# Kernel tuning notes

Hardware: AMD Instinct MI355X
Metric: run time of the kernel (lower is better)

Reference implementation:

```python
import jax, jax.numpy as jnp
import numpy as np

N_NODES = 100000
N_EDGES = 1600000
IN_CH, HID1, HID2, HID3, OUT_CH = 128, 64, 64, 256, 64


def gcn_conv(x, W, b, src, dst, n_nodes):
    """PyG GCNConv: linear transform, add self-loops, symmetric-normalized aggregation."""
    h = x @ W  # [N, d_out]
    # degree at target nodes, counting the self-loop (+1)
    deg = jnp.zeros((n_nodes,), dtype=h.dtype).at[dst].add(1.0) + 1.0
    dinv = jax.lax.rsqrt(deg)  # deg >= 1, safe
    norm = dinv[src] * dinv[dst]  # [E]
    # scatter-add normalized messages from src to dst
    agg = jnp.zeros_like(h).at[dst].add(h[src] * norm[:, None])
    # self-loop contribution: norm_ii = dinv[i]^2
    agg = agg + h * (dinv * dinv)[:, None]
    return agg + b


def setup_inputs() -> dict:
    key = jax.random.key(0)
    ks = jax.random.split(key, 8)
    x = jax.random.normal(ks[0], (N_NODES, IN_CH), dtype=jnp.float32)
    edge_index = jax.random.randint(ks[1], (2, N_EDGES), 0, N_NODES, dtype=jnp.int64)
    def glorot(k, fan_in, fan_out):
        s = jnp.sqrt(6.0 / (fan_in + fan_out)).astype(jnp.float32)
        return jax.random.uniform(k, (fan_in, fan_out), jnp.float32, -s, s)
    return {
        "x": x,
        "edge_index": edge_index,
        "W1": glorot(ks[2], IN_CH, HID1), "b1": jnp.zeros((HID1,), jnp.float32),
        "W2": glorot(ks[3], HID1, HID2), "b2": jnp.zeros((HID2,), jnp.float32),
        "W3": glorot(ks[4], HID2, HID3), "b3": jnp.zeros((HID3,), jnp.float32),
        "W4": glorot(ks[5], HID3, OUT_CH), "b4": jnp.zeros((OUT_CH,), jnp.float32),
    }


def reference(x, edge_index, W1, b1, W2, b2, W3, b3, W4, b4):
    src, dst = edge_index[0], edge_index[1]
    n = x.shape[0]
    h = jax.nn.relu(gcn_conv(x, W1, b1, src, dst, n))
    h = jax.nn.relu(gcn_conv(h, W2, b2, src, dst, n))
    h = h @ W3 + b3  # hidden Linear (no activation, per original forward)
    h = h @ W4 + b4  # output Linear
    return jax.nn.log_softmax(h, axis=-1)
```

## Files before the change

kernel.cpp:

```cpp
#include <hip/hip_runtime.h>
#include <hip/hip_bf16.h>
#include <math.h>

#define NNODES 100000
#define NEDGES 1600000
#define NB 782
#define PB 256
#define EPB 6250
#define SCAN_N (NB * PB)
#define CAP 4608

typedef __bf16 bf16x8 __attribute__((ext_vector_type(8)));
typedef float f32x4 __attribute__((ext_vector_type(4)));
typedef unsigned int u32x4 __attribute__((ext_vector_type(4)));

static __device__ inline unsigned short f2bf(float f) {
    __hip_bfloat16 h = __float2bfloat16(f);
    return *reinterpret_cast<unsigned short*>(&h);
}


__global__ __launch_bounds__(256) void hist_kernel(const int* __restrict__ dst,
                                                   int* __restrict__ histg) {
    __shared__ int h[NB];
    int tid = threadIdx.x, blk = blockIdx.x;
    for (int b = tid; b < NB; b += 256) h[b] = 0;
    __syncthreads();
    int base = blk * EPB;
    for (int i = base + tid; i < base + EPB; i += 256)
        atomicAdd(&h[dst[i] >> 7], 1);
    __syncthreads();
    for (int b = tid; b < NB; b += 256) histg[b * PB + blk] = h[b];
}


__global__ __launch_bounds__(256) void scan1_kernel(const int* __restrict__ cnt,
                                                    int* __restrict__ off,
                                                    int* __restrict__ bsum, int n) {
    __shared__ int tmp[256];
    int tid = threadIdx.x;
    int t4 = blockIdx.x * 1024 + tid * 4;
    int v0 = (t4 + 0 < n) ? cnt[t4 + 0] : 0;
    int v1 = (t4 + 1 < n) ? cnt[t4 + 1] : 0;
    int v2 = (t4 + 2 < n) ? cnt[t4 + 2] : 0;
    int v3 = (t4 + 3 < n) ? cnt[t4 + 3] : 0;
    int ssum = v0 + v1 + v2 + v3;
    tmp[tid] = ssum;
    __syncthreads();
    for (int d = 1; d < 256; d <<= 1) {
        int x = (tid >= d) ? tmp[tid - d] : 0;
        __syncthreads();
        tmp[tid] += x;
        __syncthreads();
    }
    int run = tmp[tid] - ssum;
    if (t4 + 0 < n) off[t4 + 0] = run; run += v0;
    if (t4 + 1 < n) off[t4 + 1] = run; run += v1;
    if (t4 + 2 < n) off[t4 + 2] = run; run += v2;
    if (t4 + 3 < n) off[t4 + 3] = run;
    if (tid == 255) bsum[blockIdx.x] = tmp[255];
}

__global__ __launch_bounds__(256) void scan2_kernel(const int* __restrict__ bsum,
                                                    int* __restrict__ bsum_ex, int nb) {
    __shared__ int tmp[256];
    int tid = threadIdx.x;
    int v = (tid < nb) ? bsum[tid] : 0;
    tmp[tid] = v;
    __syncthreads();
    for (int d = 1; d < 256; d <<= 1) {
        int x = (tid >= d) ? tmp[tid - d] : 0;
        __syncthreads();
        tmp[tid] += x;
        __syncthreads();
    }
    bsum_ex[tid] = tmp[tid] - v;
}

__global__ __launch_bounds__(256) void scan3t_kernel(const int* __restrict__ part_scan,
                                                     const int* __restrict__ bsum_ex,
                                                     const int* __restrict__ histg,
                                                     int* __restrict__ gbaseT,
                                                     int* __restrict__ cntT, int n) {
    int i = blockIdx.x * 256 + threadIdx.x;
    if (i < n) {
        int v = part_scan[i] + bsum_ex[i >> 10];
        int b = i >> 8, blk = i & 255;
        gbaseT[blk * NB + b] = v;
        cntT[blk * NB + b] = histg[i];
    }
}


__global__ __launch_bounds__(256) void part_kernel(const int* __restrict__ src,
                                                   const int* __restrict__ dst,
                                                   const int* __restrict__ gbaseT,
                                                   const int* __restrict__ cntT,
                                                   unsigned int* __restrict__ part) {
    __shared__ unsigned int sorted[EPB];
    __shared__ int gaddr[EPB];
    __shared__ int gcol[NB];
    __shared__ int base_l[NB];
    __shared__ int cur[NB];
    __shared__ int tmp[256];
    int tid = threadIdx.x, blk = blockIdx.x;
    for (int b = tid; b < NB; b += 256) {
        gcol[b] = gbaseT[blk * NB + b];
        base_l[b] = cntT[blk * NB + b];
        cur[b] = 0;
    }
    __syncthreads();
    int t4 = tid * 4;
    int v0 = (t4 + 0 < NB) ? base_l[t4 + 0] : 0;
    int v1 = (t4 + 1 < NB) ? base_l[t4 + 1] : 0;
    int v2 = (t4 + 2 < NB) ? base_l[t4 + 2] : 0;
    int v3 = (t4 + 3 < NB) ? base_l[t4 + 3] : 0;
    int ssum = v0 + v1 + v2 + v3;
    tmp[tid] = ssum;
    __syncthreads();
    for (int d = 1; d < 256; d <<= 1) {
        int x = (tid >= d) ? tmp[tid - d] : 0;
        __syncthreads();
        tmp[tid] += x;
        __syncthreads();
    }
    int run = tmp[tid] - ssum;
    if (t4 + 0 < NB) base_l[t4 + 0] = run; run += v0;
    if (t4 + 1 < NB) base_l[t4 + 1] = run; run += v1;
    if (t4 + 2 < NB) base_l[t4 + 2] = run; run += v2;
    if (t4 + 3 < NB) base_l[t4 + 3] = run;
    __syncthreads();
    int base = blk * EPB;
    for (int i = base + tid; i < base + EPB; i += 256) {
        int s = src[i], d = dst[i];
        int bkt = d >> 7;
        int r = atomicAdd(&cur[bkt], 1);
        int pos = base_l[bkt] + r;
        sorted[pos] = ((unsigned int)(d & 127) << 17) | (unsigned int)s;
        gaddr[pos] = gcol[bkt] + r;
    }
    __syncthreads();
    for (int i = tid; i < EPB; i += 256)
        part[gaddr[i]] = sorted[i];
}


__global__ __launch_bounds__(256) void csr_kernel(const unsigned int* __restrict__ part,
                                                  const int* __restrict__ gbaseT,
                                                  int* __restrict__ csr,
                                                  int* __restrict__ cnt_g,
                                                  int* __restrict__ off_g,
                                                  float* __restrict__ dinv_g, int n) {
    __shared__ unsigned int stage[CAP];
    __shared__ int hist2[128];
    __shared__ int sc[128];
    __shared__ int excl[128];
    __shared__ int cur2[128];
    int tid = threadIdx.x, b = blockIdx.x;
    int S = gbaseT[b];
    int T = (b == NB - 1) ? NEDGES : gbaseT[b + 1];
    int len = T - S;
    bool fit = (len <= CAP);
    if (tid < 128) { hist2[tid] = 0; cur2[tid] = 0; }
    __syncthreads();
    for (int i = tid; i < len; i += 256) {
        unsigned int p = part[S + i];
        if (fit) stage[i] = p;
        atomicAdd(&hist2[p >> 17], 1);
    }
    __syncthreads();
    if (tid < 128) sc[tid] = hist2[tid];
    __syncthreads();
    for (int d = 1; d < 128; d <<= 1) {
        int x = 0;
        if (tid < 128 && tid >= d) x = sc[tid - d];
        __syncthreads();
        if (tid < 128) sc[tid] += x;
        __syncthreads();
    }
    if (tid < 128) {
        int c = hist2[tid];
        int ex = sc[tid] - c;
        excl[tid] = ex;
        int node = b * 128 + tid;
        if (node < n) {
            cnt_g[node] = c;
            off_g[node] = S + ex;
            dinv_g[node] = rsqrtf((float)c + 1.0f);
        }
    }
    __syncthreads();
    for (int i = tid; i < len; i += 256) {
        unsigned int p = fit ? stage[i] : part[S + i];
        int dl = p >> 17;
        int s = (int)(p & 0x1FFFFu);
        int r = atomicAdd(&cur2[dl], 1);
        csr[S + excl[dl] + r] = s;
    }
}


static __device__ inline int packidx64(int k, int ch) {
    int s = k >> 5, r5 = k & 31, q = r5 >> 3, ii = r5 & 7;
    int t = ch >> 4, lo = ch & 15;
    int lane = q * 16 + lo;
    return ((t * 2 + s) * 64 + lane) * 8 + ii;
}

__global__ __launch_bounds__(256) void prep_kernel(const float* __restrict__ W1,
                                                   const float* __restrict__ W2,
                                                   const float* __restrict__ W3,
                                                   const float* __restrict__ W4,
                                                   const float* __restrict__ b3,
                                                   const float* __restrict__ b4,
                                                   unsigned short* __restrict__ Wp1,
                                                   unsigned short* __restrict__ Wp2,
                                                   unsigned short* __restrict__ Wp34,
                                                   float* __restrict__ b34,
                                                   unsigned short* __restrict__ hp) {
    int blk = blockIdx.x, tid = threadIdx.x;
    if (blk < 32) {
        int idx = blk * 256 + tid;
        int i = idx & 7, rest = idx >> 3;
        int lane = rest & 63; rest >>= 6;
        int s = rest % 4, t = rest / 4;
        int k = s * 32 + (lane >> 4) * 8 + i;
        int ch = t * 16 + (lane & 15);
        Wp1[idx] = f2bf(W1[k * 64 + ch]);
    } else if (blk < 48) {
        int idx = (blk - 32) * 256 + tid;
        int i = idx & 7, rest = idx >> 3;
        int lane = rest & 63; rest >>= 6;
        int s = rest % 2, t = rest / 2;
        int k = s * 32 + (lane >> 4) * 8 + i;
        int ch = t * 16 + (lane & 15);
        Wp2[idx] = f2bf(W2[k * 64 + ch]);
    } else if (blk == 48) {
        if (tid < 64) hp[(size_t)NNODES * 64 + tid] = 0;
    } else if (blk < 65) {
        int i = (blk - 49) * 4 + (tid >> 6);
        int j = tid & 63;
        float a = 0.f;
        for (int k = 0; k < 256; ++k) a = fmaf(W3[i * 256 + k], W4[k * 64 + j], a);
        Wp34[packidx64(i, j)] = f2bf(a);
    } else {
        if (tid < 64) {
            int j = tid;
            float a = b4[j];
            for (int k = 0; k < 256; ++k) a = fmaf(b3[k], W4[k * 64 + j], a);
            b34[j] = a;
        }
    }
}


template <int K, bool LSM, bool F32IN>
__global__ __launch_bounds__(256) void gemm_mfma_kernel(const unsigned short* __restrict__ Xb,
                                                        const float* __restrict__ Xf,
                                                        const unsigned short* __restrict__ Wp,
                                                        const float* __restrict__ bias,
                                                        const float* __restrict__ dinv,
                                                        unsigned short* __restrict__ outb,
                                                        float* __restrict__ outf, int n) {
    constexpr int S = K / 32;
    int w = threadIdx.x >> 6, lane = threadIdx.x & 63;
    int q = lane >> 4, lo = lane & 15;
    int base = blockIdx.x * 64 + w * 16;
    int nodeA = base + lo;
    int na = nodeA < n ? nodeA : 0;

    f32x4 acc[4] = {};
#pragma unroll
    for (int s = 0; s < S; ++s) {
        bf16x8 a;
        if (F32IN) {
            const float* xr = Xf + (size_t)na * K + q * 8 + s * 32;
            float4 u = *(const float4*)(xr);
            float4 v = *(const float4*)(xr + 4);
            a[0] = (__bf16)u.x; a[1] = (__bf16)u.y; a[2] = (__bf16)u.z; a[3] = (__bf16)u.w;
            a[4] = (__bf16)v.x; a[5] = (__bf16)v.y; a[6] = (__bf16)v.z; a[7] = (__bf16)v.w;
        } else {
            a = *(const bf16x8*)(Xb + (size_t)na * K + q * 8 + s * 32);
        }
#pragma unroll
        for (int t = 0; t < 4; ++t) {
            bf16x8 b = *(const bf16x8*)(Wp + ((size_t)(t * S + s) * 64 + lane) * 8);
            acc[t] = __builtin_amdgcn_mfma_f32_16x16x32_bf16(a, b, acc[t], 0, 0, 0);
        }
    }

    if (!LSM) {
#pragma unroll
        for (int r = 0; r < 4; ++r) {
            int node = base + q * 4 + r;
            if (node < n) {
                float di = dinv[node];
#pragma unroll
                for (int t = 0; t < 4; ++t)
                    outb[(size_t)node * 64 + t * 16 + lo] = f2bf(acc[t][r] * di);
            }
        }
    } else {
#pragma unroll
        for (int r = 0; r < 4; ++r) {
            int node = base + q * 4 + r;
            float v0 = acc[0][r] + bias[0 * 16 + lo];
            float v1 = acc[1][r] + bias[1 * 16 + lo];
            float v2 = acc[2][r] + bias[2 * 16 + lo];
            float v3 = acc[3][r] + bias[3 * 16 + lo];
            float mx = fmaxf(fmaxf(v0, v1), fmaxf(v2, v3));
            for (int d = 1; d < 16; d <<= 1) mx = fmaxf(mx, __shfl_xor(mx, d));
            float sm = __expf(v0 - mx) + __expf(v1 - mx) + __expf(v2 - mx) + __expf(v3 - mx);
            for (int d = 1; d < 16; d <<= 1) sm += __shfl_xor(sm, d);
            float lse = mx + __logf(sm);
            if (node < n) {
                outf[(size_t)node * 64 + 0 * 16 + lo] = v0 - lse;
                outf[(size_t)node * 64 + 1 * 16 + lo] = v1 - lse;
                outf[(size_t)node * 64 + 2 * 16 + lo] = v2 - lse;
                outf[(size_t)node * 64 + 3 * 16 + lo] = v3 - lse;
            }
        }
    }
}


__global__ __launch_bounds__(256) void aggregate_kernel(const unsigned short* __restrict__ hp,
                                                        const int* __restrict__ csr,
                                                        const int* __restrict__ off,
                                                        const int* __restrict__ cnt,
                                                        const float* __restrict__ dinv,
                                                        const float* __restrict__ bias,
                                                        unsigned short* __restrict__ out, int n) {
    int node = (blockIdx.x * 256 + threadIdx.x) >> 3;
    int cl = threadIdx.x & 7;
    if (node >= n) return;
    int c8 = cl * 8;
    int s = off[node];
    int c = cnt[node];
    const int* cp = csr + s;

    float acc0[8];
    float acc1[8] = {};
    {
        bf16x8 sv = *(const bf16x8*)(hp + (size_t)node * 64 + c8);
        u32x4 su = __builtin_bit_cast(u32x4, sv);
#pragma unroll
        for (int k = 0; k < 4; ++k) {
            acc0[2 * k]     = __builtin_bit_cast(float, su[k] << 16);
            acc0[2 * k + 1] = __builtin_bit_cast(float, su[k] & 0xFFFF0000u);
        }
    }

    int n0 = 0, n1 = 0;
    if (c > 0) n0 = cp[0];
    if (c > 1) n1 = cp[1];
    int j = 0;
    for (; j + 2 <= c; j += 2) {
        bf16x8 va = *(const bf16x8*)(hp + (size_t)n0 * 64 + c8);
        bf16x8 vb = *(const bf16x8*)(hp + (size_t)n1 * 64 + c8);
        if (j + 3 < c)      { n0 = cp[j + 2]; n1 = cp[j + 3]; }
        else if (j + 2 < c) { n0 = cp[j + 2]; }
        u32x4 ua = __builtin_bit_cast(u32x4, va);
        u32x4 ub = __builtin_bit_cast(u32x4, vb);
#pragma unroll
        for (int k = 0; k < 4; ++k) {
            acc0[2 * k]     += __builtin_bit_cast(float, ua[k] << 16);
            acc0[2 * k + 1] += __builtin_bit_cast(float, ua[k] & 0xFFFF0000u);
            acc1[2 * k]     += __builtin_bit_cast(float, ub[k] << 16);
            acc1[2 * k + 1] += __builtin_bit_cast(float, ub[k] & 0xFFFF0000u);
        }
    }
    if (j < c) {
        bf16x8 va = *(const bf16x8*)(hp + (size_t)n0 * 64 + c8);
        u32x4 ua = __builtin_bit_cast(u32x4, va);
#pragma unroll
        for (int k = 0; k < 4; ++k) {
            acc0[2 * k]     += __builtin_bit_cast(float, ua[k] << 16);
            acc0[2 * k + 1] += __builtin_bit_cast(float, ua[k] & 0xFFFF0000u);
        }
    }

    float di = dinv[node];
    float4 bv0 = *(const float4*)(bias + c8);
    float4 bv1 = *(const float4*)(bias + c8 + 4);
    float bb[8] = {bv0.x, bv0.y, bv0.z, bv0.w, bv1.x, bv1.y, bv1.z, bv1.w};
    unsigned short ov[8];
#pragma unroll
    for (int k = 0; k < 8; ++k)
        ov[k] = f2bf(fmaxf(fmaf(acc0[k] + acc1[k], di, bb[k]), 0.f));
    *(ushort4*)(out + (size_t)node * 64 + c8)     = make_ushort4(ov[0], ov[1], ov[2], ov[3]);
    *(ushort4*)(out + (size_t)node * 64 + c8 + 4) = make_ushort4(ov[4], ov[5], ov[6], ov[7]);
}


extern "C" void kernel_launch(void* const* d_in, const int* in_sizes, int n_in,
                              void* d_out, int out_size, void* d_ws, size_t ws_size,
                              hipStream_t stream) {
    const float* x  = (const float*)d_in[0];
    const int*   ei = (const int*)d_in[1];
    const float* W1 = (const float*)d_in[2];
    const float* b1 = (const float*)d_in[3];
    const float* W2 = (const float*)d_in[4];
    const float* b2 = (const float*)d_in[5];
    const float* W3 = (const float*)d_in[6];
    const float* b3 = (const float*)d_in[7];
    const float* W4 = (const float*)d_in[8];
    const float* b4 = (const float*)d_in[9];
    float* outp = (float*)d_out;

    const int N = NNODES;
    const int E = NEDGES;
    const int* srcp = ei;
    const int* dstp = ei + E;

    char* w = (char*)d_ws;
    size_t o = 0;
    auto alloc = [&](size_t bytes) { size_t r = o; o = (o + bytes + 255) & ~(size_t)255; return r; };
    size_t cnt_off   = alloc((size_t)N * 4);
    size_t off_off   = alloc((size_t)N * 4);
    size_t dinv_off  = alloc((size_t)N * 4);
    size_t histg_off = alloc((size_t)SCAN_N * 4);
    size_t gscan_off = alloc((size_t)SCAN_N * 4);
    size_t gbT_off   = alloc((size_t)SCAN_N * 4);
    size_t cntT_off  = alloc((size_t)SCAN_N * 4);
    size_t bs_off    = alloc(256 * 4);
    size_t bse_off   = alloc(256 * 4);
    size_t part_off  = alloc((size_t)E * 4);
    size_t csr_off   = alloc((size_t)E * 4);
    size_t hp_off    = alloc((size_t)(N + 1) * 64 * 2);
    size_t abf_off   = alloc((size_t)N * 64 * 2);
    size_t wp1_off   = alloc(128 * 64 * 2);
    size_t wp2_off   = alloc(64 * 64 * 2);
    size_t wp34_off  = alloc(64 * 64 * 2);
    size_t b34_off   = alloc(64 * 4);

    int*            cnt   = (int*)(w + cnt_off);
    int*            off   = (int*)(w + off_off);
    float*          dinv  = (float*)(w + dinv_off);
    int*            histg = (int*)(w + histg_off);
    int*            gscan = (int*)(w + gscan_off);
    int*            gbT   = (int*)(w + gbT_off);
    int*            cntT  = (int*)(w + cntT_off);
    int*            bs    = (int*)(w + bs_off);
    int*            bse   = (int*)(w + bse_off);
    unsigned int*   part  = (unsigned int*)(w + part_off);
    int*            csr   = (int*)(w + csr_off);
    unsigned short* hp    = (unsigned short*)(w + hp_off);
    unsigned short* abf   = (unsigned short*)(w + abf_off);
    unsigned short* Wp1   = (unsigned short*)(w + wp1_off);
    unsigned short* Wp2   = (unsigned short*)(w + wp2_off);
    unsigned short* Wp34  = (unsigned short*)(w + wp34_off);
    float*          b34   = (float*)(w + b34_off);

    const int sb = (SCAN_N + 1023) / 1024;
    const int s3b = (SCAN_N + 255) / 256;

    hist_kernel<<<PB, 256, 0, stream>>>(dstp, histg);
    scan1_kernel<<<sb, 256, 0, stream>>>(histg, gscan, bs, SCAN_N);
    scan2_kernel<<<1, 256, 0, stream>>>(bs, bse, sb);
    scan3t_kernel<<<s3b, 256, 0, stream>>>(gscan, bse, histg, gbT, cntT, SCAN_N);
    part_kernel<<<PB, 256, 0, stream>>>(srcp, dstp, gbT, cntT, part);
    csr_kernel<<<NB, 256, 0, stream>>>(part, gbT, csr, cnt, off, dinv, N);

    prep_kernel<<<66, 256, 0, stream>>>(W1, W2, W3, W4, b3, b4, Wp1, Wp2, Wp34, b34, hp);

    const int gb = (N + 63) / 64;
    const int ab = (N * 8 + 255) / 256;

    gemm_mfma_kernel<128, false, true><<<gb, 256, 0, stream>>>(nullptr, x, Wp1, nullptr, dinv, hp, nullptr, N);
    aggregate_kernel<<<ab, 256, 0, stream>>>(hp, csr, off, cnt, dinv, b1, abf, N);
    gemm_mfma_kernel<64, false, false><<<gb, 256, 0, stream>>>(abf, nullptr, Wp2, nullptr, dinv, hp, nullptr, N);
    aggregate_kernel<<<ab, 256, 0, stream>>>(hp, csr, off, cnt, dinv, b2, abf, N);
    gemm_mfma_kernel<64, true, false><<<gb, 256, 0, stream>>>(abf, nullptr, Wp34, b34, nullptr, nullptr, outp, N);
}
```

Measured before the change: 256.1 us.

## Fuse graph preprocessing, GEMMs and aggregation into fewer kernels

```diff
diff --git a/kernel.cpp b/kernel.cpp
--- a/kernel.cpp
+++ b/kernel.cpp
@@ -9,10 +9,12 @@
 #define EPB 6250
 #define SCAN_N (NB * PB)
 #define CAP 4608
+#define HTS 72
 
 typedef __bf16 bf16x8 __attribute__((ext_vector_type(8)));
 typedef float f32x4 __attribute__((ext_vector_type(4)));
 typedef unsigned int u32x4 __attribute__((ext_vector_type(4)));
+typedef unsigned short u16x8 __attribute__((ext_vector_type(8)));
 
 static __device__ inline unsigned short f2bf(float f) {
     __hip_bfloat16 h = __float2bfloat16(f);
@@ -20,17 +22,71 @@
 }
 
 
-__global__ __launch_bounds__(256) void hist_kernel(const int* __restrict__ dst,
-                                                   int* __restrict__ histg) {
+static __device__ inline int packidx64(int k, int ch) {
+    int s = k >> 5, r5 = k & 31, q = r5 >> 3, ii = r5 & 7;
+    int t = ch >> 4, lo = ch & 15;
+    int lane = q * 16 + lo;
+    return ((t * 2 + s) * 64 + lane) * 8 + ii;
+}
+
+__global__ __launch_bounds__(256) void histprep_kernel(const int* __restrict__ dst,
+                                                       int* __restrict__ histg,
+                                                       const float* __restrict__ W1,
+                                                       const float* __restrict__ W2,
+                                                       const float* __restrict__ W3,
+                                                       const float* __restrict__ W4,
+                                                       const float* __restrict__ b3,
+                                                       const float* __restrict__ b4,
+                                                       unsigned short* __restrict__ Wp1,
+                                                       unsigned short* __restrict__ Wp2,
+                                                       unsigned short* __restrict__ Wp34,
+                                                       float* __restrict__ b34,
+                                                       unsigned short* __restrict__ hp) {
     __shared__ int h[NB];
     int tid = threadIdx.x, blk = blockIdx.x;
-    for (int b = tid; b < NB; b += 256) h[b] = 0;
-    __syncthreads();
-    int base = blk * EPB;
-    for (int i = base + tid; i < base + EPB; i += 256)
-        atomicAdd(&h[dst[i] >> 7], 1);
-    __syncthreads();
-    for (int b = tid; b < NB; b += 256) histg[b * PB + blk] = h[b];
+    if (blk < PB) {
+        for (int b = tid; b < NB; b += 256) h[b] = 0;
+        __syncthreads();
+        int base = blk * EPB;
+        for (int i = base + tid; i < base + EPB; i += 256)
+            atomicAdd(&h[dst[i] >> 7], 1);
+        __syncthreads();
+        for (int b = tid; b < NB; b += 256) histg[b * PB + blk] = h[b];
+        return;
+    }
+    int pb = blk - PB;
+    if (pb < 32) {
+        int idx = pb * 256 + tid;
+        int i = idx & 7, rest = idx >> 3;
+        int lane = rest & 63; rest >>= 6;
+        int s = rest % 4, t = rest / 4;
+        int k = s * 32 + (lane >> 4) * 8 + i;
+        int ch = t * 16 + (lane & 15);
+        Wp1[idx] = f2bf(W1[k * 64 + ch]);
+    } else if (pb < 48) {
+        int idx = (pb - 32) * 256 + tid;
+        int i = idx & 7, rest = idx >> 3;
+        int lane = rest & 63; rest >>= 6;
+        int s = rest % 2, t = rest / 2;
+        int k = s * 32 + (lane >> 4) * 8 + i;
+        int ch = t * 16 + (lane & 15);
+        Wp2[idx] = f2bf(W2[k * 64 + ch]);
+    } else if (pb == 48) {
+        if (tid < 64) hp[(size_t)NNODES * 64 + tid] = 0;
+    } else if (pb < 65) {
+        int i = (pb - 49) * 4 + (tid >> 6);
+        int j = tid & 63;
+        float a = 0.f;
+        for (int k = 0; k < 256; ++k) a = fmaf(W3[i * 256 + k], W4[k * 64 + j], a);
+        Wp34[packidx64(i, j)] = f2bf(a);
+    } else {
+        if (tid < 64) {
+            int j = tid;
+            float a = b4[j];
+            for (int k = 0; k < 256; ++k) a = fmaf(b3[k], W4[k * 64 + j], a);
+            b34[j] = a;
+        }
+    }
 }
 
 
@@ -61,9 +117,13 @@
     if (tid == 255) bsum[blockIdx.x] = tmp[255];
 }
 
-__global__ __launch_bounds__(256) void scan2_kernel(const int* __restrict__ bsum,
-                                                    int* __restrict__ bsum_ex, int nb) {
+__global__ __launch_bounds__(256) void scan23t_kernel(const int* __restrict__ part_scan,
+                                                      const int* __restrict__ bsum,
+                                                      const int* __restrict__ histg,
+                                                      int* __restrict__ gbaseT,
+                                                      int* __restrict__ cntT, int n, int nb) {
     __shared__ int tmp[256];
+    __shared__ int bse[256];
     int tid = threadIdx.x;
     int v = (tid < nb) ? bsum[tid] : 0;
     tmp[tid] = v;
@@ -74,19 +134,13 @@
         tmp[tid] += x;
         __syncthreads();
     }
-    bsum_ex[tid] = tmp[tid] - v;
-}
-
-__global__ __launch_bounds__(256) void scan3t_kernel(const int* __restrict__ part_scan,
-                                                     const int* __restrict__ bsum_ex,
-                                                     const int* __restrict__ histg,
-                                                     int* __restrict__ gbaseT,
-                                                     int* __restrict__ cntT, int n) {
-    int i = blockIdx.x * 256 + threadIdx.x;
+    bse[tid] = tmp[tid] - v;
+    __syncthreads();
+    int i = blockIdx.x * 256 + tid;
     if (i < n) {
-        int v = part_scan[i] + bsum_ex[i >> 10];
+        int val = part_scan[i] + bse[i >> 10];
         int b = i >> 8, blk = i & 255;
-        gbaseT[blk * NB + b] = v;
+        gbaseT[blk * NB + b] = val;
         cntT[blk * NB + b] = histg[i];
     }
 }
@@ -145,17 +199,21 @@
 }
 
 
-__global__ __launch_bounds__(256) void csr_kernel(const unsigned int* __restrict__ part,
-                                                  const int* __restrict__ gbaseT,
-                                                  int* __restrict__ csr,
-                                                  int* __restrict__ cnt_g,
-                                                  int* __restrict__ off_g,
-                                                  float* __restrict__ dinv_g, int n) {
+__global__ __launch_bounds__(256) void csrgemm_kernel(const unsigned int* __restrict__ part,
+                                                      const int* __restrict__ gbaseT,
+                                                      const float* __restrict__ x,
+                                                      const unsigned short* __restrict__ Wp1,
+                                                      int* __restrict__ csr,
+                                                      int* __restrict__ cnt_g,
+                                                      int* __restrict__ off_g,
+                                                      float* __restrict__ dinv_g,
+                                                      unsigned short* __restrict__ hp, int n) {
     __shared__ unsigned int stage[CAP];
     __shared__ int hist2[128];
     __shared__ int sc[128];
     __shared__ int excl[128];
     __shared__ int cur2[128];
+    __shared__ float sdinv[128];
     int tid = threadIdx.x, b = blockIdx.x;
     int S = gbaseT[b];
     int T = (b == NB - 1) ? NEDGES : gbaseT[b + 1];
@@ -172,21 +230,23 @@
     if (tid < 128) sc[tid] = hist2[tid];
     __syncthreads();
     for (int d = 1; d < 128; d <<= 1) {
-        int x = 0;
-        if (tid < 128 && tid >= d) x = sc[tid - d];
-        __syncthreads();
-        if (tid < 128) sc[tid] += x;
+        int x2 = 0;
+        if (tid < 128 && tid >= d) x2 = sc[tid - d];
+        __syncthreads();
+        if (tid < 128) sc[tid] += x2;
         __syncthreads();
     }
     if (tid < 128) {
         int c = hist2[tid];
         int ex = sc[tid] - c;
         excl[tid] = ex;
+        float dv = rsqrtf((float)c + 1.0f);
+        sdinv[tid] = dv;
         int node = b * 128 + tid;
         if (node < n) {
             cnt_g[node] = c;
             off_g[node] = S + ex;
-            dinv_g[node] = rsqrtf((float)c + 1.0f);
+            dinv_g[node] = dv;
         }
     }
     __syncthreads();
@@ -197,199 +257,164 @@
         int r = atomicAdd(&cur2[dl], 1);
         csr[S + excl[dl] + r] = s;
     }
-}
-
-
-static __device__ inline int packidx64(int k, int ch) {
-    int s = k >> 5, r5 = k & 31, q = r5 >> 3, ii = r5 & 7;
-    int t = ch >> 4, lo = ch & 15;
-    int lane = q * 16 + lo;
-    return ((t * 2 + s) * 64 + lane) * 8 + ii;
-}
-
-__global__ __launch_bounds__(256) void prep_kernel(const float* __restrict__ W1,
-                                                   const float* __restrict__ W2,
-                                                   const float* __restrict__ W3,
-                                                   const float* __restrict__ W4,
-                                                   const float* __restrict__ b3,
-                                                   const float* __restrict__ b4,
-                                                   unsigned short* __restrict__ Wp1,
-                                                   unsigned short* __restrict__ Wp2,
-                                                   unsigned short* __restrict__ Wp34,
-                                                   float* __restrict__ b34,
-                                                   unsigned short* __restrict__ hp) {
-    int blk = blockIdx.x, tid = threadIdx.x;
-    if (blk < 32) {
-        int idx = blk * 256 + tid;
-        int i = idx & 7, rest = idx >> 3;
-        int lane = rest & 63; rest >>= 6;
-        int s = rest % 4, t = rest / 4;
-        int k = s * 32 + (lane >> 4) * 8 + i;
-        int ch = t * 16 + (lane & 15);
-        Wp1[idx] = f2bf(W1[k * 64 + ch]);
-    } else if (blk < 48) {
-        int idx = (blk - 32) * 256 + tid;
-        int i = idx & 7, rest = idx >> 3;
-        int lane = rest & 63; rest >>= 6;
-        int s = rest % 2, t = rest / 2;
-        int k = s * 32 + (lane >> 4) * 8 + i;
-        int ch = t * 16 + (lane & 15);
-        Wp2[idx] = f2bf(W2[k * 64 + ch]);
-    } else if (blk == 48) {
-        if (tid < 64) hp[(size_t)NNODES * 64 + tid] = 0;
-    } else if (blk < 65) {
-        int i = (blk - 49) * 4 + (tid >> 6);
-        int j = tid & 63;
-        float a = 0.f;
-        for (int k = 0; k < 256; ++k) a = fmaf(W3[i * 256 + k], W4[k * 64 + j], a);
-        Wp34[packidx64(i, j)] = f2bf(a);
-    } else {
-        if (tid < 64) {
-            int j = tid;
-            float a = b4[j];
-            for (int k = 0; k < 256; ++k) a = fmaf(b3[k], W4[k * 64 + j], a);
-            b34[j] = a;
-        }
-    }
-}
-
-
-template <int K, bool LSM, bool F32IN>
-__global__ __launch_bounds__(256) void gemm_mfma_kernel(const unsigned short* __restrict__ Xb,
-                                                        const float* __restrict__ Xf,
-                                                        const unsigned short* __restrict__ Wp,
-                                                        const float* __restrict__ bias,
-                                                        const float* __restrict__ dinv,
-                                                        unsigned short* __restrict__ outb,
-                                                        float* __restrict__ outf, int n) {
-    constexpr int S = K / 32;
-    int w = threadIdx.x >> 6, lane = threadIdx.x & 63;
+    int wv = tid >> 6, lane = tid & 63;
     int q = lane >> 4, lo = lane & 15;
-    int base = blockIdx.x * 64 + w * 16;
-    int nodeA = base + lo;
-    int na = nodeA < n ? nodeA : 0;
-
-    f32x4 acc[4] = {};
-#pragma unroll
-    for (int s = 0; s < S; ++s) {
-        bf16x8 a;
-        if (F32IN) {
-            const float* xr = Xf + (size_t)na * K + q * 8 + s * 32;
+#pragma unroll
+    for (int t2 = 0; t2 < 2; ++t2) {
+        int nl0 = wv * 32 + t2 * 16;
+        int nodeA = b * 128 + nl0 + lo;
+        int na = nodeA < n ? nodeA : 0;
+        f32x4 acc[4] = {};
+#pragma unroll
+        for (int s = 0; s < 4; ++s) {
+            const float* xr = x + (size_t)na * 128 + q * 8 + s * 32;
             float4 u = *(const float4*)(xr);
             float4 v = *(const float4*)(xr + 4);
+            bf16x8 a;
             a[0] = (__bf16)u.x; a[1] = (__bf16)u.y; a[2] = (__bf16)u.z; a[3] = (__bf16)u.w;
             a[4] = (__bf16)v.x; a[5] = (__bf16)v.y; a[6] = (__bf16)v.z; a[7] = (__bf16)v.w;
+#pragma unroll
+            for (int t = 0; t < 4; ++t) {
+                bf16x8 bfr = *(const bf16x8*)(Wp1 + ((size_t)(t * 4 + s) * 64 + lane) * 8);
+                acc[t] = __builtin_amdgcn_mfma_f32_16x16x32_bf16(a, bfr, acc[t], 0, 0, 0);
+            }
+        }
+#pragma unroll
+        for (int r = 0; r < 4; ++r) {
+            int nl = nl0 + q * 4 + r;
+            int node = b * 128 + nl;
+            if (node < n) {
+                float di = sdinv[nl];
+#pragma unroll
+                for (int t = 0; t < 4; ++t)
+                    hp[(size_t)node * 64 + t * 16 + lo] = f2bf(acc[t][r] * di);
+            }
+        }
+    }
+}
+
+
+template <bool LSM>
+__global__ __launch_bounds__(256) void aggfuse_kernel(const unsigned short* __restrict__ hsrc,
+                                                      const int* __restrict__ csr,
+                                                      const int* __restrict__ off,
+                                                      const int* __restrict__ cnt,
+                                                      const float* __restrict__ dinv,
+                                                      const float* __restrict__ biasA,
+                                                      const unsigned short* __restrict__ Wp,
+                                                      const float* __restrict__ biasB,
+                                                      unsigned short* __restrict__ outb,
+                                                      float* __restrict__ outf, int n) {
+    __shared__ __align__(16) unsigned short ht[128 * HTS];
+    int tid = threadIdx.x, b = blockIdx.x;
+    int g = tid >> 3, cl = tid & 7, c8 = cl * 8;
+    float4 bv0 = *(const float4*)(biasA + c8);
+    float4 bv1 = *(const float4*)(biasA + c8 + 4);
+    float bb[8] = {bv0.x, bv0.y, bv0.z, bv0.w, bv1.x, bv1.y, bv1.z, bv1.w};
+#pragma unroll 1
+    for (int i = 0; i < 4; ++i) {
+        int nl = g * 4 + i;
+        int node = b * 128 + nl;
+        u16x8 hv;
+#pragma unroll
+        for (int k = 0; k < 8; ++k) hv[k] = 0;
+        if (node < n) {
+            int s = off[node];
+            int c = cnt[node];
+            const int* cp = csr + s;
+            float acc0[8];
+            float acc1[8] = {};
+            bf16x8 sv = *(const bf16x8*)(hsrc + (size_t)node * 64 + c8);
+            u32x4 su = __builtin_bit_cast(u32x4, sv);
+#pragma unroll
+            for (int k = 0; k < 4; ++k) {
+                acc0[2 * k]     = __builtin_bit_cast(float, su[k] << 16);
+                acc0[2 * k + 1] = __builtin_bit_cast(float, su[k] & 0xFFFF0000u);
+            }
+            int n0 = 0, n1 = 0;
+            if (c > 0) n0 = cp[0];
+            if (c > 1) n1 = cp[1];
+            int j = 0;
+            for (; j + 2 <= c; j += 2) {
+                bf16x8 va = *(const bf16x8*)(hsrc + (size_t)n0 * 64 + c8);
+                bf16x8 vb = *(const bf16x8*)(hsrc + (size_t)n1 * 64 + c8);
+                if (j + 3 < c)      { n0 = cp[j + 2]; n1 = cp[j + 3]; }
+                else if (j + 2 < c) { n0 = cp[j + 2]; }
+                u32x4 ua = __builtin_bit_cast(u32x4, va);
+                u32x4 ub = __builtin_bit_cast(u32x4, vb);
+#pragma unroll
+                for (int k = 0; k < 4; ++k) {
+                    acc0[2 * k]     += __builtin_bit_cast(float, ua[k] << 16);
+                    acc0[2 * k + 1] += __builtin_bit_cast(float, ua[k] & 0xFFFF0000u);
+                    acc1[2 * k]     += __builtin_bit_cast(float, ub[k] << 16);
+                    acc1[2 * k + 1] += __builtin_bit_cast(float, ub[k] & 0xFFFF0000u);
+                }
+            }
+            if (j < c) {
+                bf16x8 va = *(const bf16x8*)(hsrc + (size_t)n0 * 64 + c8);
+                u32x4 ua = __builtin_bit_cast(u32x4, va);
+#pragma unroll
+                for (int k = 0; k < 4; ++k) {
+                    acc0[2 * k]     += __builtin_bit_cast(float, ua[k] << 16);
+                    acc0[2 * k + 1] += __builtin_bit_cast(float, ua[k] & 0xFFFF0000u);
+                }
+            }
+            float di = dinv[node];
+#pragma unroll
+            for (int k = 0; k < 8; ++k)
+                hv[k] = f2bf(fmaxf(fmaf(acc0[k] + acc1[k], di, bb[k]), 0.f));
+        }
+        *(u16x8*)(&ht[nl * HTS + c8]) = hv;
+    }
+    __syncthreads();
+    int wv = tid >> 6, lane = tid & 63;
+    int q = lane >> 4, lo = lane & 15;
+#pragma unroll
+    for (int t2 = 0; t2 < 2; ++t2) {
+        int nl0 = wv * 32 + t2 * 16;
+        f32x4 acc[4] = {};
+#pragma unroll
+        for (int s = 0; s < 2; ++s) {
+            bf16x8 a = *(const bf16x8*)(&ht[(nl0 + lo) * HTS + s * 32 + q * 8]);
+#pragma unroll
+            for (int t = 0; t < 4; ++t) {
+                bf16x8 bfr = *(const bf16x8*)(Wp + ((size_t)(t * 2 + s) * 64 + lane) * 8);
+                acc[t] = __builtin_amdgcn_mfma_f32_16x16x32_bf16(a, bfr, acc[t], 0, 0, 0);
+            }
+        }
+        if (!LSM) {
+#pragma unroll
+            for (int r = 0; r < 4; ++r) {
+                int node = b * 128 + nl0 + q * 4 + r;
+                if (node < n) {
+                    float di = dinv[node];
+#pragma unroll
+                    for (int t = 0; t < 4; ++t)
+                        outb[(size_t)node * 64 + t * 16 + lo] = f2bf(acc[t][r] * di);
+                }
+            }
         } else {
-            a = *(const bf16x8*)(Xb + (size_t)na * K + q * 8 + s * 32);
-        }
-#pragma unroll
-        for (int t = 0; t < 4; ++t) {
-            bf16x8 b = *(const bf16x8*)(Wp + ((size_t)(t * S + s) * 64 + lane) * 8);
-            acc[t] = __builtin_amdgcn_mfma_f32_16x16x32_bf16(a, b, acc[t], 0, 0, 0);
-        }
-    }
-
-    if (!LSM) {
-#pragma unroll
-        for (int r = 0; r < 4; ++r) {
-            int node = base + q * 4 + r;
-            if (node < n) {
-                float di = dinv[node];
-#pragma unroll
-                for (int t = 0; t < 4; ++t)
-                    outb[(size_t)node * 64 + t * 16 + lo] = f2bf(acc[t][r] * di);
-            }
-        }
-    } else {
-#pragma unroll
-        for (int r = 0; r < 4; ++r) {
-            int node = base + q * 4 + r;
-            float v0 = acc[0][r] + bias[0 * 16 + lo];
-            float v1 = acc[1][r] + bias[1 * 16 + lo];
-            float v2 = acc[2][r] + bias[2 * 16 + lo];
-            float v3 = acc[3][r] + bias[3 * 16 + lo];
-            float mx = fmaxf(fmaxf(v0, v1), fmaxf(v2, v3));
-            for (int d = 1; d < 16; d <<= 1) mx = fmaxf(mx, __shfl_xor(mx, d));
-            float sm = __expf(v0 - mx) + __expf(v1 - mx) + __expf(v2 - mx) + __expf(v3 - mx);
-            for (int d = 1; d < 16; d <<= 1) sm += __shfl_xor(sm, d);
-            float lse = mx + __logf(sm);
-            if (node < n) {
-                outf[(size_t)node * 64 + 0 * 16 + lo] = v0 - lse;
-                outf[(size_t)node * 64 + 1 * 16 + lo] = v1 - lse;
-                outf[(size_t)node * 64 + 2 * 16 + lo] = v2 - lse;
-                outf[(size_t)node * 64 + 3 * 16 + lo] = v3 - lse;
-            }
-        }
-    }
-}
-
-
-__global__ __launch_bounds__(256) void aggregate_kernel(const unsigned short* __restrict__ hp,
-                                                        const int* __restrict__ csr,
-                                                        const int* __restrict__ off,
-                                                        const int* __restrict__ cnt,
-                                                        const float* __restrict__ dinv,
-                                                        const float* __restrict__ bias,
-                                                        unsigned short* __restrict__ out, int n) {
-    int node = (blockIdx.x * 256 + threadIdx.x) >> 3;
-    int cl = threadIdx.x & 7;
-    if (node >= n) return;
-    int c8 = cl * 8;
-    int s = off[node];
-    int c = cnt[node];
-    const int* cp = csr + s;
-
-    float acc0[8];
-    float acc1[8] = {};
-    {
-        bf16x8 sv = *(const bf16x8*)(hp + (size_t)node * 64 + c8);
-        u32x4 su = __builtin_bit_cast(u32x4, sv);
-#pragma unroll
-        for (int k = 0; k < 4; ++k) {
-            acc0[2 * k]     = __builtin_bit_cast(float, su[k] << 16);
-            acc0[2 * k + 1] = __builtin_bit_cast(float, su[k] & 0xFFFF0000u);
-        }
-    }
-
-    int n0 = 0, n1 = 0;
-    if (c > 0) n0 = cp[0];
-    if (c > 1) n1 = cp[1];
-    int j = 0;
-    for (; j + 2 <= c; j += 2) {
-        bf16x8 va = *(const bf16x8*)(hp + (size_t)n0 * 64 + c8);
-        bf16x8 vb = *(const bf16x8*)(hp + (size_t)n1 * 64 + c8);
-        if (j + 3 < c)      { n0 = cp[j + 2]; n1 = cp[j + 3]; }
-        else if (j + 2 < c) { n0 = cp[j + 2]; }
-        u32x4 ua = __builtin_bit_cast(u32x4, va);
-        u32x4 ub = __builtin_bit_cast(u32x4, vb);
-#pragma unroll
-        for (int k = 0; k < 4; ++k) {
-            acc0[2 * k]     += __builtin_bit_cast(float, ua[k] << 16);
-            acc0[2 * k + 1] += __builtin_bit_cast(float, ua[k] & 0xFFFF0000u);
-            acc1[2 * k]     += __builtin_bit_cast(float, ub[k] << 16);
-            acc1[2 * k + 1] += __builtin_bit_cast(float, ub[k] & 0xFFFF0000u);
-        }
-    }
-    if (j < c) {
-        bf16x8 va = *(const bf16x8*)(hp + (size_t)n0 * 64 + c8);
-        u32x4 ua = __builtin_bit_cast(u32x4, va);
-#pragma unroll
-        for (int k = 0; k < 4; ++k) {
-            acc0[2 * k]     += __builtin_bit_cast(float, ua[k] << 16);
-            acc0[2 * k + 1] += __builtin_bit_cast(float, ua[k] & 0xFFFF0000u);
-        }
-    }
-
-    float di = dinv[node];
-    float4 bv0 = *(const float4*)(bias + c8);
-    float4 bv1 = *(const float4*)(bias + c8 + 4);
-    float bb[8] = {bv0.x, bv0.y, bv0.z, bv0.w, bv1.x, bv1.y, bv1.z, bv1.w};
-    unsigned short ov[8];
-#pragma unroll
-    for (int k = 0; k < 8; ++k)
-        ov[k] = f2bf(fmaxf(fmaf(acc0[k] + acc1[k], di, bb[k]), 0.f));
-    *(ushort4*)(out + (size_t)node * 64 + c8)     = make_ushort4(ov[0], ov[1], ov[2], ov[3]);
-    *(ushort4*)(out + (size_t)node * 64 + c8 + 4) = make_ushort4(ov[4], ov[5], ov[6], ov[7]);
+#pragma unroll
+            for (int r = 0; r < 4; ++r) {
+                int node = b * 128 + nl0 + q * 4 + r;
+                float v0 = acc[0][r] + biasB[0 * 16 + lo];
+                float v1 = acc[1][r] + biasB[1 * 16 + lo];
+                float v2 = acc[2][r] + biasB[2 * 16 + lo];
+                float v3 = acc[3][r] + biasB[3 * 16 + lo];
+                float mx = fmaxf(fmaxf(v0, v1), fmaxf(v2, v3));
+                for (int d = 1; d < 16; d <<= 1) mx = fmaxf(mx, __shfl_xor(mx, d));
+                float sm = __expf(v0 - mx) + __expf(v1 - mx) + __expf(v2 - mx) + __expf(v3 - mx);
+                for (int d = 1; d < 16; d <<= 1) sm += __shfl_xor(sm, d);
+                float lse = mx + __logf(sm);
+                if (node < n) {
+                    outf[(size_t)node * 64 + 0 * 16 + lo] = v0 - lse;
+                    outf[(size_t)node * 64 + 1 * 16 + lo] = v1 - lse;
+                    outf[(size_t)node * 64 + 2 * 16 + lo] = v2 - lse;
+                    outf[(size_t)node * 64 + 3 * 16 + lo] = v3 - lse;
+                }
+            }
+        }
+    }
 }
 
 
@@ -424,7 +449,6 @@
     size_t gbT_off   = alloc((size_t)SCAN_N * 4);
     size_t cntT_off  = alloc((size_t)SCAN_N * 4);
     size_t bs_off    = alloc(256 * 4);
-    size_t bse_off   = alloc(256 * 4);
     size_t part_off  = alloc((size_t)E * 4);
     size_t csr_off   = alloc((size_t)E * 4);
     size_t hp_off    = alloc((size_t)(N + 1) * 64 * 2);
@@ -442,7 +466,6 @@
     int*            gbT   = (int*)(w + gbT_off);
     int*            cntT  = (int*)(w + cntT_off);
     int*            bs    = (int*)(w + bs_off);
-    int*            bse   = (int*)(w + bse_off);
     unsigned int*   part  = (unsigned int*)(w + part_off);
     int*            csr   = (int*)(w + csr_off);
     unsigned short* hp    = (unsigned short*)(w + hp_off);
@@ -455,21 +478,15 @@
     const int sb = (SCAN_N + 1023) / 1024;
     const int s3b = (SCAN_N + 255) / 256;
 
-    hist_kernel<<<PB, 256, 0, stream>>>(dstp, histg);
+    histprep_kernel<<<PB + 66, 256, 0, stream>>>(dstp, histg, W1, W2, W3, W4, b3, b4,
+                                                 Wp1, Wp2, Wp34, b34, hp);
     scan1_kernel<<<sb, 256, 0, stream>>>(histg, gscan, bs, SCAN_N);
-    scan2_kernel<<<1, 256, 0, stream>>>(bs, bse, sb);
-    scan3t_kernel<<<s3b, 256, 0, stream>>>(gscan, bse, histg, gbT, cntT, SCAN_N);
+    scan23t_kernel<<<s3b, 256, 0, stream>>>(gscan, bs, histg, gbT, cntT, SCAN_N, sb);
     part_kernel<<<PB, 256, 0, stream>>>(srcp, dstp, gbT, cntT, part);
-    csr_kernel<<<NB, 256, 0, stream>>>(part, gbT, csr, cnt, off, dinv, N);
-
-    prep_kernel<<<66, 256, 0, stream>>>(W1, W2, W3, W4, b3, b4, Wp1, Wp2, Wp34, b34, hp);
-
-    const int gb = (N + 63) / 64;
-    const int ab = (N * 8 + 255) / 256;
-
-    gemm_mfma_kernel<128, false, true><<<gb, 256, 0, stream>>>(nullptr, x, Wp1, nullptr, dinv, hp, nullptr, N);
-    aggregate_kernel<<<ab, 256, 0, stream>>>(hp, csr, off, cnt, dinv, b1, abf, N);
-    gemm_mfma_kernel<64, false, false><<<gb, 256, 0, stream>>>(abf, nullptr, Wp2, nullptr, dinv, hp, nullptr, N);
-    aggregate_kernel<<<ab, 256, 0, stream>>>(hp, csr, off, cnt, dinv, b2, abf, N);
-    gemm_mfma_kernel<64, true, false><<<gb, 256, 0, stream>>>(abf, nullptr, Wp34, b34, nullptr, nullptr, outp, N);
-}
+    csrgemm_kernel<<<NB, 256, 0, stream>>>(part, gbT, x, Wp1, csr, cnt, off, dinv, hp, N);
+
+    aggfuse_kernel<false><<<NB, 256, 0, stream>>>(hp, csr, off, cnt, dinv, b1, Wp2,
+                                                  nullptr, abf, nullptr, N);
+    aggfuse_kernel<true><<<NB, 256, 0, stream>>>(abf, csr, off, cnt, dinv, b2, Wp34,
+                                                 b34, nullptr, outp, N);
+}
```

Result: faster. 248.6 us (-2.9%).
